# Kernel optimization log

Measured on AMD Instinct MI355X. Metric: run time of the kernel, lower is better.

The kernel has to match this reference:

```python
import jax, jax.numpy as jnp
import numpy as np
from math import factorial

# ---- static config (mirrors init_kwargs) ----
ZS = np.array([1, 6, 7, 8], dtype=np.int64)
NZ = 4
N_ATOM_BASIS = 3
CHAN = N_ATOM_BASIS ** 2          # 9 edge channels
MAX_L = 3
N_RBF = 8                          # radial basis functions
N_RB = 8                           # radial embedding dim
CUTOFF = 5.5
P_CUT = 6
MP_NORM = 1.0 / 10.0 ** 0.5        # 1/sqrt(avg_num_neighbors)
NUM_MP = 1
N_NODES = 4000
N_EDGES = 48000

def _make_l_list(max_l):
    lst = []
    for l in range(max_l + 1):
        for lx in range(l, -1, -1):
            for ly in range(l - lx, -1, -1):
                lst.append((lx, ly, l - lx - ly))
    return lst

L_LIST = _make_l_list(MAX_L)       # 20 (lx,ly,lz) tuples
N_L = len(L_LIST)
L_OF = np.array([sum(t) for t in L_LIST], dtype=np.int32)
LX = np.array([t[0] for t in L_LIST])
LY = np.array([t[1] for t in L_LIST])
LZ = np.array([t[2] for t in L_LIST])
# multinomial prefactors l!/(lx!ly!lz!), grouped per l for the nu=2 symmetrizer
PREF = np.array([factorial(sum(t)) / (factorial(t[0]) * factorial(t[1]) * factorial(t[2])) for t in L_LIST], dtype=np.float32)
SYM2 = np.zeros((N_L, MAX_L + 1), dtype=np.float32)
SYM2[np.arange(N_L), L_OF] = PREF

def _bessel_rbf(r):
    # r: [E,1] -> [E, N_RBF];  e_n(r) = sqrt(2/rc) * sin(n pi r / rc) / r
    n = jnp.arange(1, N_RBF + 1, dtype=r.dtype)
    return jnp.sqrt(2.0 / CUTOFF) * jnp.sin(n * jnp.pi * r / CUTOFF) / r

def _poly_cutoff(r):
    p = float(P_CUT)
    u = r / CUTOFF
    f = 1.0 - 0.5 * (p + 1.0) * (p + 2.0) * u ** p + p * (p + 2.0) * u ** (p + 1.0) - 0.5 * p * (p + 1.0) * u ** (p + 2.0)
    return f * (u < 1.0)

def _angular(unit):
    # monomials x^lx * y^ly * z^lz of the unit edge vector -> [E, N_L]
    x, y, z = unit[:, 0:1], unit[:, 1:2], unit[:, 2:3]
    return (x ** jnp.asarray(LX)) * (y ** jnp.asarray(LY)) * (z ** jnp.asarray(LZ))

def _radial_transform(A, W_rt):
    # shared per-l linear map along radial axis: [N, N_RBF, N_L, C] -> [N, N_RB, N_L, C]
    Wg = W_rt[jnp.asarray(L_OF)]   # [N_L, N_RBF, N_RB]
    return jnp.einsum('nric,irs->nsic', A, Wg)

def _symmetrize(A):
    # nu=1: A at lxlylz=(0,0,0); nu=2, each l: sum_{|lxlylz|=l} multinomial * A^2
    B1 = A[:, :, 0:1, :]
    B2 = jnp.einsum('nric,il->nrlc', A * A, jnp.asarray(SYM2))
    return jnp.concatenate([B1, B2], axis=2)   # [N, N_RB, 1+(MAX_L+1), C]

def _forward(positions, shifts, W_emb, W_rt, W_nm, atomic_numbers, edge_index):
    sender, receiver = edge_index[0], edge_index[1]
    one_hot = (atomic_numbers[:, None] == jnp.asarray(ZS)[None, :]).astype(positions.dtype)
    node_emb = one_hot @ W_emb                                    # [N, n_atom_basis]
    # edge encoding: flattened outer product of sender/receiver embeddings -> [E, CHAN]
    enc = (node_emb[sender][:, :, None] * node_emb[receiver][:, None, :]).reshape(-1, CHAN)
    vec = positions[receiver] - positions[sender] + shifts
    lengths = jnp.linalg.norm(vec, axis=-1, keepdims=True)        # [E,1]
    unit = vec / lengths
    rc = _bessel_rbf(lengths) * _poly_cutoff(lengths)             # [E, N_RBF]
    ang = _angular(unit)                                          # [E, N_L]
    edge_attri = rc[:, :, None, None] * ang[:, None, :, None] * enc[:, None, None, :]
    A = jax.ops.segment_sum(edge_attri, receiver, num_segments=N_NODES)
    A = _radial_transform(A, W_rt)                                # [N, N_RB, N_L, C]
    B = _symmetrize(A)
    feats = [B]
    Wnm_exp = W_nm[:, :, jnp.asarray(L_OF), :]                    # expand per-l memory weights to lxlylz
    for _ in range(NUM_MP):
        memory = A * Wnm_exp                                      # NodeMemory
        chi = B.sum(axis=(1, 2))                                  # [N, C] invariant scalar per channel
        msg_B = edge_attri * chi[sender][:, None, None, :]        # MesssageBchi
        A_B = _radial_transform(jax.ops.segment_sum(msg_B, receiver, num_segments=N_NODES), W_rt)
        msg_A = A[sender] * rc[:, :, None, None]                  # MessageAr: radial-weighted sender A
        A = (A_B + jax.ops.segment_sum(msg_A, receiver, num_segments=N_NODES)) * MP_NORM + memory
        B = _symmetrize(A)
        feats.append(B)
    return jnp.stack(feats, axis=-1)                              # [N, N_RB, 5, C, 1+NUM_MP]

def setup_inputs() -> dict:
    key = jax.random.key(0)
    k = jax.random.split(key, 8)
    positions = jax.random.uniform(k[0], (N_NODES, 3), dtype=jnp.float32) * 3.0
    shifts = jnp.zeros((N_EDGES, 3), dtype=jnp.float32)
    species_idx = jax.random.randint(k[1], (N_NODES,), 0, NZ)
    atomic_numbers = jnp.asarray(ZS)[species_idx]
    sender = jax.random.randint(k[2], (N_EDGES,), 0, N_NODES)
    receiver = (sender + 1 + jax.random.randint(k[3], (N_EDGES,), 0, N_NODES - 1)) % N_NODES  # no self-edges
    edge_index = jnp.stack([sender, receiver])
    W_emb = jax.random.normal(k[4], (NZ, N_ATOM_BASIS), dtype=jnp.float32) * 0.5
    W_rt = jax.random.normal(k[5], (MAX_L + 1, N_RBF, N_RB), dtype=jnp.float32) / np.sqrt(N_RBF)
    W_nm = jax.random.uniform(k[6], (1, N_RB, MAX_L + 1, CHAN), dtype=jnp.float32)
    return {"positions": positions, "shifts": shifts, "W_emb": W_emb, "W_rt": W_rt, "W_nm": W_nm, "atomic_numbers": atomic_numbers, "edge_index": edge_index}

def reference(positions, shifts, W_emb, W_rt, W_nm, atomic_numbers, edge_index):
    return _forward(positions, shifts, W_emb, W_rt, W_nm, atomic_numbers, edge_index)
```

## Files before the change

### kernel.cpp

```cpp
#include <hip/hip_runtime.h>
#include <hip/hip_fp16.h>

#ifndef M_PIf
#define M_PIf 3.14159265358979323846f
#endif

constexpr int NNODE = 4000;
constexpr int NEDGE = 48000;
constexpr int NLA   = 20;
constexpr int NCH   = 9;
constexpr int NRB   = 8;
constexpr int NEL   = NRB * NLA * NCH;
constexpr int NP2   = NEL / 2;
constexpr int FW    = 40;
constexpr int EC    = 32;
constexpr int PF    = 16;
constexpr float CUT = 5.5f;
constexpr float MPN = 0.316227766016837933f;

__constant__ int   c_LOF[NLA]  = {0,1,1,1,2,2,2,2,2,2,3,3,3,3,3,3,3,3,3,3};
__constant__ float c_PREF[NLA] = {1,1,1,1,1,2,2,1,2,1,1,3,3,3,6,3,1,3,3,1};
__constant__ int   c_GB[4] = {0,0,1,4};
__constant__ int   c_GE[4] = {0,1,4,10};

__global__ void k_count(const int* __restrict__ ei, int* __restrict__ counts) {
  int e = blockIdx.x * blockDim.x + threadIdx.x;
  if (e >= NEDGE) return;
  atomicAdd(&counts[ei[NEDGE + e]], 1);
}

__global__ void k_scan(const int* __restrict__ counts, int* __restrict__ offsets,
                       int* __restrict__ cursor) {
  __shared__ int lds[1024];
  int t = threadIdx.x;
  int base = t*4;
  int c0 = (base+0 < NNODE) ? counts[base+0] : 0;
  int c1 = (base+1 < NNODE) ? counts[base+1] : 0;
  int c2 = (base+2 < NNODE) ? counts[base+2] : 0;
  int c3 = (base+3 < NNODE) ? counts[base+3] : 0;
  lds[t] = c0+c1+c2+c3;
  __syncthreads();
  for (int d = 1; d < 1024; d <<= 1) {
    int v = (t >= d) ? lds[t-d] : 0;
    __syncthreads();
    lds[t] += v;
    __syncthreads();
  }
  int excl = (t == 0) ? 0 : lds[t-1];
  int o0 = excl, o1 = o0+c0, o2 = o1+c1, o3 = o2+c2;
  if (base+0 < NNODE) { offsets[base+0]=o0; cursor[base+0]=o0; }
  if (base+1 < NNODE) { offsets[base+1]=o1; cursor[base+1]=o1; }
  if (base+2 < NNODE) { offsets[base+2]=o2; cursor[base+2]=o2; }
  if (base+3 < NNODE) { offsets[base+3]=o3; cursor[base+3]=o3; }
  if (t == 1023) offsets[NNODE] = lds[1023];
}

__global__ void k_edgec(const float* __restrict__ pos, const float* __restrict__ shifts,
                        const int* __restrict__ ei, const int* __restrict__ an,
                        const float* __restrict__ W_emb,
                        int* __restrict__ cursor, float* __restrict__ facS,
                        int* __restrict__ sndS) {
  int e = blockIdx.x * blockDim.x + threadIdx.x;
  if (e >= NEDGE) return;
  int snd = ei[e];
  int rcv = ei[NEDGE + e];
  float vx = pos[rcv*3+0] - pos[snd*3+0] + shifts[e*3+0];
  float vy = pos[rcv*3+1] - pos[snd*3+1] + shifts[e*3+1];
  float vz = pos[rcv*3+2] - pos[snd*3+2] + shifts[e*3+2];
  float len = sqrtf(vx*vx + vy*vy + vz*vz);
  float inv = 1.0f / len;
  float x = vx*inv, y = vy*inv, z = vz*inv;
  float u  = len * (1.0f/CUT);
  float u2 = u*u;
  float u6 = u2*u2*u2;
  float fcut = 1.0f - 28.0f*u6 + 48.0f*u6*u - 21.0f*u6*u2;
  if (u >= 1.0f) fcut = 0.0f;
  float pre = sqrtf(2.0f/CUT) * fcut * inv;
  int p = atomicAdd(&cursor[rcv], 1);
  float* f = facS + (size_t)p*FW;
  #pragma unroll
  for (int j = 0; j < NRB; ++j)
    f[j] = pre * sinf((float)(j+1) * M_PIf * u);
  float ang[NLA];
  ang[0]=1.0f; ang[1]=x; ang[2]=y; ang[3]=z;
  ang[4]=x*x; ang[5]=x*y; ang[6]=x*z; ang[7]=y*y; ang[8]=y*z; ang[9]=z*z;
  ang[10]=ang[4]*x; ang[11]=ang[4]*y; ang[12]=ang[4]*z;
  ang[13]=x*ang[7]; ang[14]=ang[5]*z; ang[15]=x*ang[9];
  ang[16]=ang[7]*y; ang[17]=ang[7]*z; ang[18]=y*ang[9]; ang[19]=ang[9]*z;
  #pragma unroll
  for (int i = 0; i < NLA; ++i) f[8+i] = ang[i];
  int as_ = an[snd], ar_ = an[rcv];
  int sps = (as_==1)?0:(as_==6)?1:(as_==7)?2:3;
  int spr = (ar_==1)?0:(ar_==6)?1:(ar_==7)?2:3;
  float es0=W_emb[sps*3+0], es1=W_emb[sps*3+1], es2=W_emb[sps*3+2];
  float er0=W_emb[spr*3+0], er1=W_emb[spr*3+1], er2=W_emb[spr*3+2];
  f[28]=es0*er0; f[29]=es0*er1; f[30]=es0*er2;
  f[31]=es1*er0; f[32]=es1*er1; f[33]=es1*er2;
  f[34]=es2*er0; f[35]=es2*er1; f[36]=es2*er2;
  f[37]=0.f; f[38]=0.f; f[39]=0.f;
  sndS[p] = snd;
}


__global__ __launch_bounds__(256, 4) void k_nodeA(
    const float* __restrict__ facS, const int* __restrict__ offsets,
    const float* __restrict__ W_rt,
    float2* __restrict__ A1f2, __half2* __restrict__ A1h2,
    float* __restrict__ chi, float* __restrict__ out) {
  __shared__ float s_wrt[256];
  __shared__ float s_e[EC*FW];
  __shared__ float s_tile[8*90];
  __shared__ float s_B[288];
  int bid = blockIdx.x;
  int n = bid >> 1, half = bid & 1;
  int t = threadIdx.x;
  s_wrt[t] = W_rt[t];
  int rq[2], kk[2], i0[2], c0[2], l0[2], i1[2], c1[2], l1[2], qg[2];
  bool val[2];
  #pragma unroll
  for (int jj = 0; jj < 2; ++jj) {
    int j = t + jj*256;
    val[jj] = (j < 360);
    int js = val[jj] ? j : 0;
    rq[jj] = js / 45; kk[jj] = js % 45;
    qg[jj] = rq[jj]*90 + kk[jj] + half*45;
    int rem0 = 2*(kk[jj] + 45*half);
    i0[jj] = rem0 / 9;  c0[jj] = rem0 % 9;  l0[jj] = c_LOF[i0[jj]];
    int rem1 = rem0 + 1;
    i1[jj] = rem1 / 9;  c1[jj] = rem1 % 9;  l1[jj] = c_LOF[i1[jj]];
  }
  float acc[2][2] = {{0,0},{0,0}};
  int beg = offsets[n], end = offsets[n+1];
  const float4* f4 = (const float4*)facS;
  for (int base = beg; base < end; base += EC) {
    int m = min(EC, end - base);
    __syncthreads();
    for (int idx = t; idx < m*(FW/4); idx += 256)
      ((float4*)s_e)[idx] = f4[(size_t)base*(FW/4) + idx];
    __syncthreads();
    for (int p = 0; p < m; ++p) {
      const float* e0 = s_e + p*FW;
      #pragma unroll
      for (int jj = 0; jj < 2; ++jj) {
        if (val[jj]) {
          float rv = e0[rq[jj]];
          acc[jj][0] += rv * e0[8+i0[jj]] * e0[28+c0[jj]];
          acc[jj][1] += rv * e0[8+i1[jj]] * e0[28+c1[jj]];
        }
      }
    }
  }
  __syncthreads();
  #pragma unroll
  for (int jj = 0; jj < 2; ++jj)
    if (val[jj]) {
      s_tile[rq[jj]*90 + 2*kk[jj]]     = acc[jj][0];
      s_tile[rq[jj]*90 + 2*kk[jj] + 1] = acc[jj][1];
    }
  __syncthreads();
  float a1v[2][2];
  #pragma unroll
  for (int jj = 0; jj < 2; ++jj) {
    if (val[jj]) {
      float ab0 = 0.f, ab1 = 0.f;
      #pragma unroll
      for (int r = 0; r < NRB; ++r) {
        ab0 += s_tile[r*90 + 2*kk[jj]]     * s_wrt[l0[jj]*64 + r*8 + rq[jj]];
        ab1 += s_tile[r*90 + 2*kk[jj] + 1] * s_wrt[l1[jj]*64 + r*8 + rq[jj]];
      }
      a1v[jj][0] = ab0; a1v[jj][1] = ab1;
      size_t qi = (size_t)n*NP2 + qg[jj];
      A1f2[qi] = make_float2(ab0, ab1);
      A1h2[qi] = __floats2half2_rn(ab0, ab1);
    }
  }
  __syncthreads();
  #pragma unroll
  for (int jj = 0; jj < 2; ++jj)
    if (val[jj]) {
      s_tile[rq[jj]*90 + 2*kk[jj]]     = a1v[jj][0];
      s_tile[rq[jj]*90 + 2*kk[jj] + 1] = a1v[jj][1];
    }
  __syncthreads();
  if (half == 0) {
    for (int m2 = t; m2 < 288; m2 += 256) {
      int s = m2 / 36, rm = m2 % 36, l5 = rm / 9, c = rm % 9;
      float b;
      if (l5 == 0) b = s_tile[s*90 + c];
      else {
        b = 0.f;
        for (int i = c_GB[l5]; i < c_GE[l5]; ++i) {
          float v = s_tile[s*90 + i*9 + c];
          b += c_PREF[i]*v*v;
        }
      }
      out[(size_t)(((n*8 + s)*5 + l5)*9 + c)*2 + 0] = b;
      s_B[m2] = b;
    }
    __syncthreads();
    if (t < 9) {
      float x = 0.f;
      #pragma unroll
      for (int u = 0; u < 32; ++u) x += s_B[u*9 + t];
      atomicAdd(&chi[n*9 + t], x);
    }
  } else {
    if (t < 72) {
      int s = t / 9, c = t % 9;
      float b = 0.f;
      for (int i = 10; i < 20; ++i) {
        float v = s_tile[s*90 + (i-10)*9 + c];
        b += c_PREF[i]*v*v;
      }
      out[(size_t)(((n*8 + s)*5 + 4)*9 + c)*2 + 0] = b;
      s_B[t] = b;
    }
    __syncthreads();
    if (t < 9) {
      float x = 0.f;
      #pragma unroll
      for (int u = 0; u < 8; ++u) x += s_B[u*9 + t];
      atomicAdd(&chi[n*9 + t], x);
    }
  }
}

__global__ __launch_bounds__(256, 4) void k_nodeMP(
    const float* __restrict__ facS, const int* __restrict__ offsets,
    const int* __restrict__ sndS,
    const float* __restrict__ W_rt, const float* __restrict__ W_nm,
    const float2* __restrict__ A1f2, const __half2* __restrict__ A1h2,
    const float* __restrict__ chi, float* __restrict__ out) {
  __shared__ float s_wrt[256];
  __shared__ float s_wnm[288];
  __shared__ float s_e[EC*FW];
  __shared__ float s_echi[EC*12];
  __shared__ int   s_snd[EC];
  __shared__ float s_tile[8*90];
  int bid = blockIdx.x;
  int n = bid >> 1, half = bid & 1;
  int t = threadIdx.x;
  s_wrt[t] = W_rt[t];
  s_wnm[t] = W_nm[t];
  if (t < 32) s_wnm[256 + t] = W_nm[256 + t];
  int rq[2], kk[2], i0[2], c0[2], l0[2], i1[2], c1[2], l1[2], qg[2];
  bool val[2];
  #pragma unroll
  for (int jj = 0; jj < 2; ++jj) {
    int j = t + jj*256;
    val[jj] = (j < 360);
    int js = val[jj] ? j : 0;
    rq[jj] = js / 45; kk[jj] = js % 45;
    qg[jj] = rq[jj]*90 + kk[jj] + half*45;
    int rem0 = 2*(kk[jj] + 45*half);
    i0[jj] = rem0 / 9;  c0[jj] = rem0 % 9;  l0[jj] = c_LOF[i0[jj]];
    int rem1 = rem0 + 1;
    i1[jj] = rem1 / 9;  c1[jj] = rem1 % 9;  l1[jj] = c_LOF[i1[jj]];
  }
  float accA[2][2] = {{0,0},{0,0}};
  float accB[2][2] = {{0,0},{0,0}};
  float2 mymem[2];
  #pragma unroll
  for (int jj = 0; jj < 2; ++jj)
    mymem[jj] = val[jj] ? A1f2[(size_t)n*NP2 + qg[jj]] : make_float2(0.f, 0.f);
  int beg = offsets[n], end = offsets[n+1];
  const float4* f4 = (const float4*)facS;
  for (int base = beg; base < end; base += EC) {
    int m = min(EC, end - base);
    __syncthreads();
    for (int idx = t; idx < m*(FW/4); idx += 256)
      ((float4*)s_e)[idx] = f4[(size_t)base*(FW/4) + idx];
    for (int idx = t; idx < m; idx += 256) s_snd[idx] = sndS[base + idx];
    __syncthreads();
    for (int idx = t; idx < m*9; idx += 256) {
      int p = idx / 9, c = idx - p*9;
      s_echi[p*12 + c] = chi[s_snd[p]*9 + c] * s_e[p*FW + 28 + c];
    }
    __syncthreads();
    for (int g0 = 0; g0 < m; g0 += PF) {
      int gm = min(PF, m - g0);
      __half2 ga[PF], gb[PF];
      #pragma unroll
      for (int x = 0; x < PF; ++x) {
        int pp = g0 + ((x < gm) ? x : (gm - 1));
        const __half2* Ah = A1h2 + (size_t)s_snd[pp]*NP2;
        ga[x] = Ah[qg[0]];
        if (val[1]) gb[x] = Ah[qg[1]];
      }
      #pragma unroll
      for (int x = 0; x < PF; ++x) {
        if (x < gm) {
          const float* e0 = s_e + (g0+x)*FW;
          const float* x0 = s_echi + (g0+x)*12;
          {
            float rv = e0[rq[0]];
            float2 gf = __half22float2(ga[x]);
            accA[0][0] += gf.x * rv;
            accA[0][1] += gf.y * rv;
            accB[0][0] += rv * e0[8+i0[0]] * x0[c0[0]];
            accB[0][1] += rv * e0[8+i1[0]] * x0[c1[0]];
          }
          if (val[1]) {
            float rv = e0[rq[1]];
            float2 gf = __half22float2(gb[x]);
            accA[1][0] += gf.x * rv;
            accA[1][1] += gf.y * rv;
            accB[1][0] += rv * e0[8+i0[1]] * x0[c0[1]];
            accB[1][1] += rv * e0[8+i1[1]] * x0[c1[1]];
          }
        }
      }
    }
  }
  __syncthreads();
  #pragma unroll
  for (int jj = 0; jj < 2; ++jj)
    if (val[jj]) {
      s_tile[rq[jj]*90 + 2*kk[jj]]     = accB[jj][0];
      s_tile[rq[jj]*90 + 2*kk[jj] + 1] = accB[jj][1];
    }
  __syncthreads();
  float a2v[2][2];
  #pragma unroll
  for (int jj = 0; jj < 2; ++jj) {
    if (val[jj]) {
      float ab0 = 0.f, ab1 = 0.f;
      #pragma unroll
      for (int r = 0; r < NRB; ++r) {
        ab0 += s_tile[r*90 + 2*kk[jj]]     * s_wrt[l0[jj]*64 + r*8 + rq[jj]];
        ab1 += s_tile[r*90 + 2*kk[jj] + 1] * s_wrt[l1[jj]*64 + r*8 + rq[jj]];
      }
      float mem0 = mymem[jj].x * s_wnm[rq[jj]*36 + l0[jj]*9 + c0[jj]];
      float mem1 = mymem[jj].y * s_wnm[rq[jj]*36 + l1[jj]*9 + c1[jj]];
      a2v[jj][0] = (ab0 + accA[jj][0])*MPN + mem0;
      a2v[jj][1] = (ab1 + accA[jj][1])*MPN + mem1;
    }
  }
  __syncthreads();
  #pragma unroll
  for (int jj = 0; jj < 2; ++jj)
    if (val[jj]) {
      s_tile[rq[jj]*90 + 2*kk[jj]]     = a2v[jj][0];
      s_tile[rq[jj]*90 + 2*kk[jj] + 1] = a2v[jj][1];
    }
  __syncthreads();
  if (half == 0) {
    for (int m2 = t; m2 < 288; m2 += 256) {
      int s = m2 / 36, rm = m2 % 36, l5 = rm / 9, c = rm % 9;
      float b;
      if (l5 == 0) b = s_tile[s*90 + c];
      else {
        b = 0.f;
        for (int i = c_GB[l5]; i < c_GE[l5]; ++i) {
          float v = s_tile[s*90 + i*9 + c];
          b += c_PREF[i]*v*v;
        }
      }
      out[(size_t)(((n*8 + s)*5 + l5)*9 + c)*2 + 1] = b;
    }
  } else {
    if (t < 72) {
      int s = t / 9, c = t % 9;
      float b = 0.f;
      for (int i = 10; i < 20; ++i) {
        float v = s_tile[s*90 + (i-10)*9 + c];
        b += c_PREF[i]*v*v;
      }
      out[(size_t)(((n*8 + s)*5 + 4)*9 + c)*2 + 1] = b;
    }
  }
}

extern "C" void kernel_launch(void* const* d_in, const int* in_sizes, int n_in,
                              void* d_out, int out_size, void* d_ws, size_t ws_size,
                              hipStream_t stream) {
  const float* pos    = (const float*)d_in[0];
  const float* shifts = (const float*)d_in[1];
  const float* W_emb  = (const float*)d_in[2];
  const float* W_rt   = (const float*)d_in[3];
  const float* W_nm   = (const float*)d_in[4];
  const int*   an     = (const int*)d_in[5];
  const int*   ei     = (const int*)d_in[6];
  float* out = (float*)d_out;

  char* ws = (char*)d_ws;
  size_t off = 0;
  auto carve = [&](size_t bytes) {
    void* p = ws + off;
    off = (off + bytes + 255) & ~(size_t)255;
    return p;
  };
  float*   facS    = (float*)carve((size_t)FW*NEDGE*sizeof(float));
  int*     sndS    = (int*)carve((size_t)NEDGE*sizeof(int));
  float2*  A1f2    = (float2*)carve((size_t)NNODE*NEL*sizeof(float));
  __half2* A1h2    = (__half2*)carve((size_t)NNODE*NEL*sizeof(__half));
  float*   chi     = (float*)carve((size_t)NNODE*NCH*sizeof(float));
  int*     counts  = (int*)carve((size_t)NNODE*sizeof(int));
  int*     offsets = (int*)carve((size_t)(NNODE+1)*sizeof(int));
  int*     cursor  = (int*)carve((size_t)NNODE*sizeof(int));

  size_t z0 = (size_t)((char*)chi - ws);
  size_t z1 = (size_t)((char*)counts - ws) + (size_t)NNODE*sizeof(int);
  hipMemsetAsync((char*)ws + z0, 0, z1 - z0, stream);
  k_count<<<(NEDGE+255)/256, 256, 0, stream>>>(ei, counts);
  k_scan<<<1, 1024, 0, stream>>>(counts, offsets, cursor);
  k_edgec<<<(NEDGE+255)/256, 256, 0, stream>>>(pos, shifts, ei, an, W_emb, cursor, facS, sndS);
  k_nodeA<<<NNODE*2, 256, 0, stream>>>(facS, offsets, W_rt, A1f2, A1h2, chi, out);
  k_nodeMP<<<NNODE*2, 256, 0, stream>>>(facS, offsets, sndS, W_rt, W_nm, A1f2, A1h2, chi, out);
}
```

Before: 131.5 us.

## Precompute per-edge chi products in separate kernel and shrink gather prefetch depth

Moves the per-edge product of sender chi and the species embedding into a new k_echi kernel writing a padded 12-float buffer. k_nodeMP then loads it with float4 copies, removing one barrier and the in-block chi gather. The sender-feature gather prefetch drops from 16 to 4 edges, reading sender indices straight from global memory, to cut register pressure. Launch bounds on both node kernels rise to 8 blocks per CU, trading one extra launch and buffer for fewer syncs and more occupancy, with less memory-latency hiding per wave.

```diff
diff --git a/kernel.cpp b/kernel.cpp
--- a/kernel.cpp
+++ b/kernel.cpp
@@ -14,7 +14,6 @@
 constexpr int NP2   = NEL / 2;
 constexpr int FW    = 40;
 constexpr int EC    = 32;
-constexpr int PF    = 16;
 constexpr float CUT = 5.5f;
 constexpr float MPN = 0.316227766016837933f;
 
@@ -101,8 +100,21 @@
   sndS[p] = snd;
 }
 
-
-__global__ __launch_bounds__(256, 4) void k_nodeA(
+__global__ void k_echi(const float* __restrict__ facS, const int* __restrict__ sndS,
+                       const float* __restrict__ chi, float* __restrict__ echiS) {
+  int p = blockIdx.x * blockDim.x + threadIdx.x;
+  if (p >= NEDGE) return;
+  int snd = sndS[p];
+  const float* f = facS + (size_t)p*FW;
+  float* o = echiS + (size_t)p*12;
+  #pragma unroll
+  for (int c = 0; c < 9; ++c)
+    o[c] = chi[snd*9 + c] * f[28 + c];
+  o[9] = 0.f; o[10] = 0.f; o[11] = 0.f;
+}
+
+
+__global__ __launch_bounds__(256, 8) void k_nodeA(
     const float* __restrict__ facS, const int* __restrict__ offsets,
     const float* __restrict__ W_rt,
     float2* __restrict__ A1f2, __half2* __restrict__ A1h2,
@@ -225,17 +237,16 @@
   }
 }
 
-__global__ __launch_bounds__(256, 4) void k_nodeMP(
+__global__ __launch_bounds__(256, 8) void k_nodeMP(
     const float* __restrict__ facS, const int* __restrict__ offsets,
-    const int* __restrict__ sndS,
+    const int* __restrict__ sndS, const float* __restrict__ echiS,
     const float* __restrict__ W_rt, const float* __restrict__ W_nm,
     const float2* __restrict__ A1f2, const __half2* __restrict__ A1h2,
-    const float* __restrict__ chi, float* __restrict__ out) {
+    float* __restrict__ out) {
   __shared__ float s_wrt[256];
   __shared__ float s_wnm[288];
   __shared__ float s_e[EC*FW];
-  __shared__ float s_echi[EC*12];
-  __shared__ int   s_snd[EC];
+  __shared__ float s_ec[EC*12];
   __shared__ float s_tile[8*90];
   int bid = blockIdx.x;
   int n = bid >> 1, half = bid & 1;
@@ -265,49 +276,68 @@
     mymem[jj] = val[jj] ? A1f2[(size_t)n*NP2 + qg[jj]] : make_float2(0.f, 0.f);
   int beg = offsets[n], end = offsets[n+1];
   const float4* f4 = (const float4*)facS;
+  const float4* e4 = (const float4*)echiS;
   for (int base = beg; base < end; base += EC) {
     int m = min(EC, end - base);
     __syncthreads();
     for (int idx = t; idx < m*(FW/4); idx += 256)
       ((float4*)s_e)[idx] = f4[(size_t)base*(FW/4) + idx];
-    for (int idx = t; idx < m; idx += 256) s_snd[idx] = sndS[base + idx];
-    __syncthreads();
-    for (int idx = t; idx < m*9; idx += 256) {
-      int p = idx / 9, c = idx - p*9;
-      s_echi[p*12 + c] = chi[s_snd[p]*9 + c] * s_e[p*FW + 28 + c];
-    }
-    __syncthreads();
-    for (int g0 = 0; g0 < m; g0 += PF) {
-      int gm = min(PF, m - g0);
-      __half2 ga[PF], gb[PF];
-      #pragma unroll
-      for (int x = 0; x < PF; ++x) {
-        int pp = g0 + ((x < gm) ? x : (gm - 1));
-        const __half2* Ah = A1h2 + (size_t)s_snd[pp]*NP2;
-        ga[x] = Ah[qg[0]];
-        if (val[1]) gb[x] = Ah[qg[1]];
-      }
-      #pragma unroll
-      for (int x = 0; x < PF; ++x) {
-        if (x < gm) {
-          const float* e0 = s_e + (g0+x)*FW;
-          const float* x0 = s_echi + (g0+x)*12;
-          {
-            float rv = e0[rq[0]];
-            float2 gf = __half22float2(ga[x]);
-            accA[0][0] += gf.x * rv;
-            accA[0][1] += gf.y * rv;
-            accB[0][0] += rv * e0[8+i0[0]] * x0[c0[0]];
-            accB[0][1] += rv * e0[8+i1[0]] * x0[c1[0]];
-          }
-          if (val[1]) {
-            float rv = e0[rq[1]];
-            float2 gf = __half22float2(gb[x]);
-            accA[1][0] += gf.x * rv;
-            accA[1][1] += gf.y * rv;
-            accB[1][0] += rv * e0[8+i0[1]] * x0[c0[1]];
-            accB[1][1] += rv * e0[8+i1[1]] * x0[c1[1]];
-          }
+    for (int idx = t; idx < m*3; idx += 256)
+      ((float4*)s_ec)[idx] = e4[(size_t)base*3 + idx];
+    __syncthreads();
+    int p = 0;
+    for (; p + 3 < m; p += 4) {
+      int sd0 = sndS[base+p+0], sd1 = sndS[base+p+1];
+      int sd2 = sndS[base+p+2], sd3 = sndS[base+p+3];
+      __half2 g0a = A1h2[(size_t)sd0*NP2 + qg[0]];
+      __half2 g1a = A1h2[(size_t)sd1*NP2 + qg[0]];
+      __half2 g2a = A1h2[(size_t)sd2*NP2 + qg[0]];
+      __half2 g3a = A1h2[(size_t)sd3*NP2 + qg[0]];
+      __half2 g0b, g1b, g2b, g3b;
+      if (val[1]) {
+        g0b = A1h2[(size_t)sd0*NP2 + qg[1]];
+        g1b = A1h2[(size_t)sd1*NP2 + qg[1]];
+        g2b = A1h2[(size_t)sd2*NP2 + qg[1]];
+        g3b = A1h2[(size_t)sd3*NP2 + qg[1]];
+      }
+      #pragma unroll
+      for (int x = 0; x < 4; ++x) {
+        const float* e0 = s_e + (p+x)*FW;
+        const float* x0 = s_ec + (p+x)*12;
+        __half2 ga = (x==0)?g0a:(x==1)?g1a:(x==2)?g2a:g3a;
+        {
+          float rv = e0[rq[0]];
+          float2 gf = __half22float2(ga);
+          accA[0][0] += gf.x * rv;
+          accA[0][1] += gf.y * rv;
+          accB[0][0] += rv * e0[8+i0[0]] * x0[c0[0]];
+          accB[0][1] += rv * e0[8+i1[0]] * x0[c1[0]];
+        }
+        if (val[1]) {
+          __half2 gb = (x==0)?g0b:(x==1)?g1b:(x==2)?g2b:g3b;
+          float rv = e0[rq[1]];
+          float2 gf = __half22float2(gb);
+          accA[1][0] += gf.x * rv;
+          accA[1][1] += gf.y * rv;
+          accB[1][0] += rv * e0[8+i0[1]] * x0[c0[1]];
+          accB[1][1] += rv * e0[8+i1[1]] * x0[c1[1]];
+        }
+      }
+    }
+    for (; p < m; ++p) {
+      int sd = sndS[base+p];
+      const float* e0 = s_e + p*FW;
+      const float* x0 = s_ec + p*12;
+      const __half2* Ah = A1h2 + (size_t)sd*NP2;
+      #pragma unroll
+      for (int jj = 0; jj < 2; ++jj) {
+        if (val[jj]) {
+          float rv = e0[rq[jj]];
+          float2 gf = __half22float2(Ah[qg[jj]]);
+          accA[jj][0] += gf.x * rv;
+          accA[jj][1] += gf.y * rv;
+          accB[jj][0] += rv * e0[8+i0[jj]] * x0[c0[jj]];
+          accB[jj][1] += rv * e0[8+i1[jj]] * x0[c1[jj]];
         }
       }
     }
@@ -392,6 +422,7 @@
   };
   float*   facS    = (float*)carve((size_t)FW*NEDGE*sizeof(float));
   int*     sndS    = (int*)carve((size_t)NEDGE*sizeof(int));
+  float*   echiS   = (float*)carve((size_t)12*NEDGE*sizeof(float));
   float2*  A1f2    = (float2*)carve((size_t)NNODE*NEL*sizeof(float));
   __half2* A1h2    = (__half2*)carve((size_t)NNODE*NEL*sizeof(__half));
   float*   chi     = (float*)carve((size_t)NNODE*NCH*sizeof(float));
@@ -406,5 +437,6 @@
   k_scan<<<1, 1024, 0, stream>>>(counts, offsets, cursor);
   k_edgec<<<(NEDGE+255)/256, 256, 0, stream>>>(pos, shifts, ei, an, W_emb, cursor, facS, sndS);
   k_nodeA<<<NNODE*2, 256, 0, stream>>>(facS, offsets, W_rt, A1f2, A1h2, chi, out);
-  k_nodeMP<<<NNODE*2, 256, 0, stream>>>(facS, offsets, sndS, W_rt, W_nm, A1f2, A1h2, chi, out);
-}
+  k_echi<<<(NEDGE+255)/256, 256, 0, stream>>>(facS, sndS, chi, echiS);
+  k_nodeMP<<<NNODE*2, 256, 0, stream>>>(facS, offsets, sndS, echiS, W_rt, W_nm, A1f2, A1h2, out);
+}
```

After: 122.1 us. 1.08x faster.
